# Kernel tuning notes

Measured on AMD Instinct MI355X. Metric: run time of the kernel, lower is better.

Reference implementation:

```python
import jax, jax.numpy as jnp
import numpy as np

H = 16
D_MODEL = 1024
D_K = D_MODEL // H  # 64
NEG = -1e9


def setup_inputs() -> dict:
    key = jax.random.key(0)
    ks = jax.random.split(key, 9)
    nb, nw = 4, 2048
    Q = jax.random.normal(ks[0], (nb, nw, D_MODEL), dtype=jnp.float32)
    K = jax.random.normal(ks[1], (nb, nw, D_MODEL), dtype=jnp.float32)
    V = jax.random.normal(ks[2], (nb, nw, D_MODEL), dtype=jnp.float32)
    mask = jax.random.randint(ks[3], (nb, nw, nw), 0, 2, dtype=jnp.int32)
    s = 1.0 / np.sqrt(D_MODEL)
    Wq = jax.random.normal(ks[4], (D_MODEL, D_MODEL), dtype=jnp.float32) * s
    Wk = jax.random.normal(ks[5], (D_MODEL, D_MODEL), dtype=jnp.float32) * s
    Wv = jax.random.normal(ks[6], (D_MODEL, D_MODEL), dtype=jnp.float32) * s
    Wo = jax.random.normal(ks[7], (D_MODEL, D_MODEL), dtype=jnp.float32) * s
    return {"Q": Q, "K": K, "V": V, "mask": mask,
            "Wq": Wq, "Wk": Wk, "Wv": Wv, "Wo": Wo}


def reference(Q, K, V, mask, Wq, Wk, Wv, Wo):
    nb, nw, _ = Q.shape
    scaling = jnp.asarray(np.sqrt(D_K), dtype=Q.dtype)
    # nn.Linear(bias=False): y = x @ W.T; split heads -> [nb, h, nw, d_k]
    q = (Q @ Wq.T).reshape(nb, nw, H, D_K).transpose(0, 2, 1, 3)
    k = (K @ Wk.T).reshape(nb, nw, H, D_K).transpose(0, 2, 1, 3)
    v = (V @ Wv.T).reshape(nb, nw, H, D_K).transpose(0, 2, 1, 3)
    scores = jnp.einsum('bhqd,bhkd->bhqk', q, k) / scaling
    # mask broadcast over heads (unsqueeze(1) in torch)
    scores = jnp.where(mask[:, None, :, :] == 0, jnp.asarray(NEG, scores.dtype), scores)
    probs = jax.nn.softmax(scores, axis=-1)
    # dropout is identity in eval mode
    attn = jnp.einsum('bhqk,bhkd->bhqd', probs, v)
    x = attn.transpose(0, 2, 1, 3).reshape(nb, nw, D_MODEL)
    return x @ Wo.T
```

## Files before the change

### kernel.cpp

```cpp
#include <hip/hip_runtime.h>
#include <hip/hip_bf16.h>
#include <cstdint>
#include <cmath>

#define NB 4
#define NW 2048
#define DM 1024
#define NH 16
#define DK 64

typedef __attribute__((ext_vector_type(8))) short bf16x8;
typedef __attribute__((ext_vector_type(4))) float f32x4;
union cvt8 { uint4 u; __hip_bfloat16 h[8]; };

__device__ __forceinline__ void async_ld16(const void* g, void* l) {
  __builtin_amdgcn_global_load_lds((__attribute__((address_space(1))) void*)g,
                                   (__attribute__((address_space(3))) void*)l,
                                   16, 0, 0);
}

__device__ __forceinline__ unsigned short bf16bits(float x) {
  __hip_bfloat16 h = __float2bfloat16(x);
  return *(unsigned short*)&h;
}

__global__ void __launch_bounds__(256) cvt_qkv(const float* __restrict__ Q,
                                               const float* __restrict__ K,
                                               const float* __restrict__ V,
                                               __hip_bfloat16* __restrict__ Qb,
                                               __hip_bfloat16* __restrict__ Kb,
                                               __hip_bfloat16* __restrict__ Vb) {
  const float* in = blockIdx.y == 0 ? Q : (blockIdx.y == 1 ? K : V);
  __hip_bfloat16* out = blockIdx.y == 0 ? Qb : (blockIdx.y == 1 ? Kb : Vb);
  size_t i = ((size_t)blockIdx.x * 256 + threadIdx.x) * 8;
  float4 a = *(const float4*)(in + i);
  float4 b = *(const float4*)(in + i + 4);
  cvt8 c;
#pragma unroll
  for (int t = 0; t < 4; ++t) {
    c.h[t]     = __float2bfloat16(((const float*)&a)[t]);
    c.h[4 + t] = __float2bfloat16(((const float*)&b)[t]);
  }
  *(uint4*)(out + i) = c.u;
}

__global__ void __launch_bounds__(256) cvt_w(const float* __restrict__ W0,
                                             const float* __restrict__ W1,
                                             const float* __restrict__ W2,
                                             const float* __restrict__ W3,
                                             __hip_bfloat16* __restrict__ Wb) {
  const float* in = blockIdx.y == 0 ? W0 : (blockIdx.y == 1 ? W1 : (blockIdx.y == 2 ? W2 : W3));
  __hip_bfloat16* out = Wb + (size_t)blockIdx.y * DM * DM;
  size_t i = ((size_t)blockIdx.x * 256 + threadIdx.x) * 8;
  float4 a = *(const float4*)(in + i);
  float4 b = *(const float4*)(in + i + 4);
  cvt8 c;
#pragma unroll
  for (int t = 0; t < 4; ++t) {
    c.h[t]     = __float2bfloat16(((const float*)&a)[t]);
    c.h[4 + t] = __float2bfloat16(((const float*)&b)[t]);
  }
  *(uint4*)(out + i) = c.u;
}

__global__ void __launch_bounds__(256) mask_pack(const int* __restrict__ mask,
                                                 unsigned long long* __restrict__ bits) {
  int lane = threadIdx.x & 63;
  size_t tid = (size_t)blockIdx.x * blockDim.x + threadIdx.x;
  size_t widx = tid >> 6;
  int m = mask[widx * 64 + lane];
  unsigned long long b = __ballot(m != 0);
  if (lane == 0) bits[widx] = b;
}

__global__ void __launch_bounds__(256) gemm_qkv(const __hip_bfloat16* __restrict__ Qb,
                                                const __hip_bfloat16* __restrict__ Kb,
                                                const __hip_bfloat16* __restrict__ Vb,
                                                const __hip_bfloat16* __restrict__ Wb,
                                                __hip_bfloat16* __restrict__ q_ws,
                                                __hip_bfloat16* __restrict__ k_ws,
                                                __hip_bfloat16* __restrict__ vt) {
  __shared__ __align__(16) __hip_bfloat16 sA[128 * 32];
  __shared__ __align__(16) __hip_bfloat16 sB[128 * 32];
  const int z = blockIdx.z;
  const __hip_bfloat16* A = z == 0 ? Qb : (z == 1 ? Kb : Vb);
  const __hip_bfloat16* W = Wb + (size_t)z * DM * DM;
  const int tid = threadIdx.x;
  const int lane = tid & 63;
  const int l15 = lane & 15, quad = lane >> 4;
  const int rowA = blockIdx.y * 128;
  const int colB = blockIdx.x * 128;
  const int wm = ((tid >> 6) >> 1) * 64, wn = ((tid >> 6) & 1) * 64;

  const f32x4 fz = {0.f, 0.f, 0.f, 0.f};
  f32x4 acc[4][4];
#pragma unroll
  for (int i = 0; i < 4; ++i)
#pragma unroll
    for (int j = 0; j < 4; ++j) acc[i][j] = fz;

  for (int k0 = 0; k0 < DM; k0 += 32) {
#pragma unroll
    for (int j = 0; j < 2; ++j) {
      int c = j * 256 + tid;
      int r = c >> 2, col = (c & 3) * 8;
      int ldsOff = (j * 256 + (tid & ~63)) * 16;
      async_ld16(A + (size_t)(rowA + r) * DM + k0 + col, (char*)sA + ldsOff);
      async_ld16(W + (size_t)(colB + r) * DM + k0 + col, (char*)sB + ldsOff);
    }
    __syncthreads();
    bf16x8 af[4], bfr[4];
#pragma unroll
    for (int i = 0; i < 4; ++i) {
      af[i]  = *(const bf16x8*)(sA + (wm + i * 16 + l15) * 32 + quad * 8);
      bfr[i] = *(const bf16x8*)(sB + (wn + i * 16 + l15) * 32 + quad * 8);
    }
#pragma unroll
    for (int i = 0; i < 4; ++i)
#pragma unroll
      for (int j = 0; j < 4; ++j)
        acc[i][j] = __builtin_amdgcn_mfma_f32_16x16x32_bf16(af[i], bfr[j], acc[i][j], 0, 0, 0);
    __syncthreads();
  }

  if (z < 2) {
    __hip_bfloat16* C = z == 0 ? q_ws : k_ws;
    float alpha = z == 0 ? 0.125f : 1.0f;
#pragma unroll
    for (int i = 0; i < 4; ++i) {
      int row = rowA + wm + i * 16 + quad * 4;
#pragma unroll
      for (int j = 0; j < 4; ++j) {
        int col = colB + wn + j * 16 + l15;
#pragma unroll
        for (int r = 0; r < 4; ++r)
          C[(size_t)(row + r) * DM + col] = __float2bfloat16(acc[i][j][r] * alpha);
      }
    }
  } else {
#pragma unroll
    for (int i = 0; i < 4; ++i) {
      int row = rowA + wm + i * 16 + quad * 4;
      int bb = row >> 11, tok = row & 2047;
#pragma unroll
      for (int j = 0; j < 4; ++j) {
        int col = colB + wn + j * 16 + l15;
        uint2 u;
        u.x = (unsigned int)bf16bits(acc[i][j][0]) | ((unsigned int)bf16bits(acc[i][j][1]) << 16);
        u.y = (unsigned int)bf16bits(acc[i][j][2]) | ((unsigned int)bf16bits(acc[i][j][3]) << 16);
        *(uint2*)(vt + ((size_t)bb * 1024 + col) * 2048 + tok) = u;
      }
    }
  }
}

__global__ void __launch_bounds__(256) gemm_out(const __hip_bfloat16* __restrict__ A,
                                                const __hip_bfloat16* __restrict__ W,
                                                float* __restrict__ C) {
  __shared__ __align__(16) __hip_bfloat16 sA[128 * 32];
  __shared__ __align__(16) __hip_bfloat16 sB[128 * 32];
  const int tid = threadIdx.x;
  const int lane = tid & 63;
  const int l15 = lane & 15, quad = lane >> 4;
  const int rowA = blockIdx.y * 128;
  const int colB = blockIdx.x * 128;
  const int wm = ((tid >> 6) >> 1) * 64, wn = ((tid >> 6) & 1) * 64;

  const f32x4 fz = {0.f, 0.f, 0.f, 0.f};
  f32x4 acc[4][4];
#pragma unroll
  for (int i = 0; i < 4; ++i)
#pragma unroll
    for (int j = 0; j < 4; ++j) acc[i][j] = fz;

  for (int k0 = 0; k0 < DM; k0 += 32) {
#pragma unroll
    for (int j = 0; j < 2; ++j) {
      int c = j * 256 + tid;
      int r = c >> 2, col = (c & 3) * 8;
      int ldsOff = (j * 256 + (tid & ~63)) * 16;
      async_ld16(A + (size_t)(rowA + r) * DM + k0 + col, (char*)sA + ldsOff);
      async_ld16(W + (size_t)(colB + r) * DM + k0 + col, (char*)sB + ldsOff);
    }
    __syncthreads();
    bf16x8 af[4], bfr[4];
#pragma unroll
    for (int i = 0; i < 4; ++i) {
      af[i]  = *(const bf16x8*)(sA + (wm + i * 16 + l15) * 32 + quad * 8);
      bfr[i] = *(const bf16x8*)(sB + (wn + i * 16 + l15) * 32 + quad * 8);
    }
#pragma unroll
    for (int i = 0; i < 4; ++i)
#pragma unroll
      for (int j = 0; j < 4; ++j)
        acc[i][j] = __builtin_amdgcn_mfma_f32_16x16x32_bf16(af[i], bfr[j], acc[i][j], 0, 0, 0);
    __syncthreads();
  }
#pragma unroll
  for (int i = 0; i < 4; ++i) {
    int row = rowA + wm + i * 16 + quad * 4;
#pragma unroll
    for (int j = 0; j < 4; ++j) {
      int col = colB + wn + j * 16 + l15;
#pragma unroll
      for (int r = 0; r < 4; ++r)
        C[(size_t)(row + r) * DM + col] = acc[i][j][r];
    }
  }
}

#define LDSK 72

__global__ void __launch_bounds__(256) attn_fused(const __hip_bfloat16* __restrict__ q,
                                                  const __hip_bfloat16* __restrict__ kk,
                                                  const __hip_bfloat16* __restrict__ vt,
                                                  const unsigned long long* __restrict__ mbits,
                                                  __hip_bfloat16* __restrict__ o) {
  __shared__ __align__(16) __hip_bfloat16 sK[64 * LDSK];
  __shared__ __align__(16) __hip_bfloat16 sVT[64 * LDSK];
  __shared__ __align__(16) __hip_bfloat16 sP[4][16 * LDSK];

  const int tid = threadIdx.x;
  const int wave = tid >> 6, lane = tid & 63;
  const int l15 = lane & 15, quad = lane >> 4;
  const int b = blockIdx.z, h = blockIdx.y;
  const int qbase = blockIdx.x * 64 + wave * 16;

  const __hip_bfloat16* qp = q + (size_t)(b * NW + qbase + l15) * DM + h * DK + quad * 8;
  bf16x8 aq0 = *(const bf16x8*)qp;
  bf16x8 aq1 = *(const bf16x8*)(qp + 32);

  const __hip_bfloat16* vbase = vt + ((size_t)b * 1024 + h * DK) * 2048;

  const f32x4 fz = {0.f, 0.f, 0.f, 0.f};
  f32x4 oacc[4];
  float ls[4] = {0.f, 0.f, 0.f, 0.f};
#pragma unroll
  for (int i = 0; i < 4; ++i) oacc[i] = fz;

  for (int kt = 0; kt < NW / 64; ++kt) {
    __syncthreads();
#pragma unroll
    for (int j = 0; j < 2; ++j) {
      int c = j * 256 + tid;
      int r = c >> 3, col = (c & 7) * 8;
      *(uint4*)(sK + r * LDSK + col) =
          *(const uint4*)(kk + (size_t)(b * NW + kt * 64 + r) * DM + h * DK + col);
      *(uint4*)(sVT + r * LDSK + col) =
          *(const uint4*)(vbase + (size_t)r * 2048 + kt * 64 + col);
    }
    unsigned long long mw[4];
#pragma unroll
    for (int r = 0; r < 4; ++r)
      mw[r] = mbits[(size_t)(b * NW + qbase + quad * 4 + r) * (NW / 64) + kt];
    __syncthreads();

    f32x4 S[4];
#pragma unroll
    for (int nc = 0; nc < 4; ++nc) {
      bf16x8 b0 = *(const bf16x8*)(sK + (nc * 16 + l15) * LDSK + quad * 8);
      bf16x8 b1 = *(const bf16x8*)(sK + (nc * 16 + l15) * LDSK + 32 + quad * 8);
      f32x4 t = fz;
      t = __builtin_amdgcn_mfma_f32_16x16x32_bf16(aq0, b0, t, 0, 0, 0);
      t = __builtin_amdgcn_mfma_f32_16x16x32_bf16(aq1, b1, t, 0, 0, 0);
      S[nc] = t;
    }
    unsigned long long sh[4];
#pragma unroll
    for (int r = 0; r < 4; ++r) sh[r] = mw[r] >> l15;
#pragma unroll
    for (int nc = 0; nc < 4; ++nc)
#pragma unroll
      for (int r = 0; r < 4; ++r) {
        float p = __expf(S[nc][r]);
        if (!((sh[r] >> (nc * 16)) & 1ull)) p = 0.f;
        ls[r] += p;
        sP[wave][(quad * 4 + r) * LDSK + nc * 16 + l15] = __float2bfloat16(p);
      }
    __threadfence_block();

    bf16x8 ap0 = *(const bf16x8*)(&sP[wave][l15 * LDSK + quad * 8]);
    bf16x8 ap1 = *(const bf16x8*)(&sP[wave][l15 * LDSK + 32 + quad * 8]);
#pragma unroll
    for (int nc = 0; nc < 4; ++nc) {
      bf16x8 b0 = *(const bf16x8*)(sVT + (nc * 16 + l15) * LDSK + quad * 8);
      bf16x8 b1 = *(const bf16x8*)(sVT + (nc * 16 + l15) * LDSK + 32 + quad * 8);
      oacc[nc] = __builtin_amdgcn_mfma_f32_16x16x32_bf16(ap0, b0, oacc[nc], 0, 0, 0);
      oacc[nc] = __builtin_amdgcn_mfma_f32_16x16x32_bf16(ap1, b1, oacc[nc], 0, 0, 0);
    }
  }

#pragma unroll
  for (int s = 1; s < 16; s <<= 1)
#pragma unroll
    for (int r = 0; r < 4; ++r) ls[r] += __shfl_xor(ls[r], s, 64);

  float inv[4];
#pragma unroll
  for (int r = 0; r < 4; ++r) inv[r] = 1.0f / fmaxf(ls[r], 1e-30f);
#pragma unroll
  for (int nc = 0; nc < 4; ++nc)
#pragma unroll
    for (int r = 0; r < 4; ++r)
      o[(size_t)(b * NW + qbase + quad * 4 + r) * DM + h * DK + nc * 16 + l15] =
          __float2bfloat16(oacc[nc][r] * inv[r]);
}

extern "C" void kernel_launch(void* const* d_in, const int* in_sizes, int n_in,
                              void* d_out, int out_size, void* d_ws, size_t ws_size,
                              hipStream_t stream) {
  const float* Q  = (const float*)d_in[0];
  const float* K  = (const float*)d_in[1];
  const float* V  = (const float*)d_in[2];
  const int*   Mm = (const int*)d_in[3];
  const float* Wq = (const float*)d_in[4];
  const float* Wk = (const float*)d_in[5];
  const float* Wv = (const float*)d_in[6];
  const float* Wo = (const float*)d_in[7];
  float* out = (float*)d_out;

  char* ws = (char*)d_ws;
  const size_t tb = (size_t)NB * NW * DM * sizeof(__hip_bfloat16);
  const size_t wb = (size_t)DM * DM * sizeof(__hip_bfloat16);
  __hip_bfloat16* Qb   = (__hip_bfloat16*)(ws);
  __hip_bfloat16* Kb   = (__hip_bfloat16*)(ws + tb);
  __hip_bfloat16* k_ws = (__hip_bfloat16*)(ws + 2 * tb);
  __hip_bfloat16* vt   = (__hip_bfloat16*)(ws + 3 * tb);
  __hip_bfloat16* Wb   = (__hip_bfloat16*)(ws + 4 * tb);
  unsigned long long* mbits = (unsigned long long*)(ws + 4 * tb + 4 * wb);
  __hip_bfloat16* q_ws = (__hip_bfloat16*)d_out;
  __hip_bfloat16* Vb   = (__hip_bfloat16*)((char*)d_out + tb);
  __hip_bfloat16* a_ws = Qb;

  const int gq = (int)((size_t)NB * NW * DM / 8 / 256);
  const int gw = (int)((size_t)DM * DM / 8 / 256);

  mask_pack<<<(size_t)NB * NW * NW / 256, 256, 0, stream>>>(Mm, mbits);
  cvt_qkv<<<dim3(gq, 3), 256, 0, stream>>>(Q, K, V, Qb, Kb, Vb);
  cvt_w<<<dim3(gw, 4), 256, 0, stream>>>(Wq, Wk, Wv, Wo, Wb);
  gemm_qkv<<<dim3(DM / 128, NB * NW / 128, 3), 256, 0, stream>>>(Qb, Kb, Vb, Wb,
                                                                 q_ws, k_ws, vt);
  attn_fused<<<dim3(NW / 64, NH, NB), 256, 0, stream>>>(q_ws, k_ws, vt, mbits, a_ws);
  gemm_out<<<dim3(DM / 128, NB * NW / 128), 256, 0, stream>>>(a_ws, Wb + 3 * (size_t)DM * DM, out);
}
```

Before: 477.6 us.

## Compute transposed scores and pass P to PV MFMA via permlane swaps instead of LDS

Swaps the MFMA operand order so the S tile comes out transposed, which leaves each lane holding probabilities for one query row. The P fragments for the PV MFMA are then rebuilt in registers with v_permlane32/16_swap, removing the per-wave sP LDS round trip and the fence. The mask bitmap is re-laid out as [b][kt][row] so each lane loads one coalesced word. Exponentials use the native v_exp_f32 with log2(e) folded into the q scaling. The row-sum reduction is restructured to match the new layout, and correctness depends on the permlane lane mapping matching the MFMA A-operand layout.

Measured after the change: 480.2 us. About the same (+0.5%).

```diff
diff --git a/kernel.cpp b/kernel.cpp
--- a/kernel.cpp
+++ b/kernel.cpp
@@ -12,6 +12,7 @@
 typedef __attribute__((ext_vector_type(8))) short bf16x8;
 typedef __attribute__((ext_vector_type(4))) float f32x4;
 union cvt8 { uint4 u; __hip_bfloat16 h[8]; };
+union pk2 { unsigned u; unsigned short s[2]; };
 
 __device__ __forceinline__ void async_ld16(const void* g, void* l) {
   __builtin_amdgcn_global_load_lds((__attribute__((address_space(1))) void*)g,
@@ -22,6 +23,12 @@
 __device__ __forceinline__ unsigned short bf16bits(float x) {
   __hip_bfloat16 h = __float2bfloat16(x);
   return *(unsigned short*)&h;
+}
+
+__device__ __forceinline__ float exp2_fast(float x) {
+  float r;
+  asm("v_exp_f32 %0, %1" : "=v"(r) : "v"(x));
+  return r;
 }
 
 __global__ void __launch_bounds__(256) cvt_qkv(const float* __restrict__ Q,
@@ -69,8 +76,13 @@
   size_t tid = (size_t)blockIdx.x * blockDim.x + threadIdx.x;
   size_t widx = tid >> 6;
   int m = mask[widx * 64 + lane];
-  unsigned long long b = __ballot(m != 0);
-  if (lane == 0) bits[widx] = b;
+  unsigned long long bm = __ballot(m != 0);
+  if (lane == 0) {
+    int kt  = (int)(widx & 31);
+    int row = (int)((widx >> 5) & 2047);
+    int bb  = (int)(widx >> 16);
+    bits[((size_t)bb * 32 + kt) * NW + row] = bm;
+  }
 }
 
 __global__ void __launch_bounds__(256) gemm_qkv(const __hip_bfloat16* __restrict__ Qb,
@@ -125,7 +137,7 @@
 
   if (z < 2) {
     __hip_bfloat16* C = z == 0 ? q_ws : k_ws;
-    float alpha = z == 0 ? 0.125f : 1.0f;
+    float alpha = z == 0 ? 0.18033688011112042f : 1.0f;
 #pragma unroll
     for (int i = 0; i < 4; ++i) {
       int row = rowA + wm + i * 16 + quad * 4;
@@ -214,11 +226,10 @@
 __global__ void __launch_bounds__(256) attn_fused(const __hip_bfloat16* __restrict__ q,
                                                   const __hip_bfloat16* __restrict__ kk,
                                                   const __hip_bfloat16* __restrict__ vt,
-                                                  const unsigned long long* __restrict__ mbits,
+                                                  const unsigned long long* __restrict__ mbt,
                                                   __hip_bfloat16* __restrict__ o) {
   __shared__ __align__(16) __hip_bfloat16 sK[64 * LDSK];
   __shared__ __align__(16) __hip_bfloat16 sVT[64 * LDSK];
-  __shared__ __align__(16) __hip_bfloat16 sP[4][16 * LDSK];
 
   const int tid = threadIdx.x;
   const int wave = tid >> 6, lane = tid & 63;
@@ -231,12 +242,13 @@
   bf16x8 aq1 = *(const bf16x8*)(qp + 32);
 
   const __hip_bfloat16* vbase = vt + ((size_t)b * 1024 + h * DK) * 2048;
+  const unsigned long long* mrow = mbt + (size_t)b * 32 * NW + qbase + l15;
 
   const f32x4 fz = {0.f, 0.f, 0.f, 0.f};
   f32x4 oacc[4];
-  float ls[4] = {0.f, 0.f, 0.f, 0.f};
 #pragma unroll
   for (int i = 0; i < 4; ++i) oacc[i] = fz;
+  float lsr[4] = {0.f, 0.f, 0.f, 0.f};
 
   for (int kt = 0; kt < NW / 64; ++kt) {
     __syncthreads();
@@ -249,55 +261,67 @@
       *(uint4*)(sVT + r * LDSK + col) =
           *(const uint4*)(vbase + (size_t)r * 2048 + kt * 64 + col);
     }
-    unsigned long long mw[4];
-#pragma unroll
-    for (int r = 0; r < 4; ++r)
-      mw[r] = mbits[(size_t)(b * NW + qbase + quad * 4 + r) * (NW / 64) + kt];
-    __syncthreads();
-
-    f32x4 S[4];
+    unsigned long long mw = mrow[(size_t)kt * NW];
+    __syncthreads();
+
+    unsigned long long msh = mw >> (quad * 4);
+    unsigned int u[4][2];
 #pragma unroll
     for (int nc = 0; nc < 4; ++nc) {
-      bf16x8 b0 = *(const bf16x8*)(sK + (nc * 16 + l15) * LDSK + quad * 8);
-      bf16x8 b1 = *(const bf16x8*)(sK + (nc * 16 + l15) * LDSK + 32 + quad * 8);
+      bf16x8 kf0 = *(const bf16x8*)(sK + (nc * 16 + l15) * LDSK + quad * 8);
+      bf16x8 kf1 = *(const bf16x8*)(sK + (nc * 16 + l15) * LDSK + 32 + quad * 8);
       f32x4 t = fz;
-      t = __builtin_amdgcn_mfma_f32_16x16x32_bf16(aq0, b0, t, 0, 0, 0);
-      t = __builtin_amdgcn_mfma_f32_16x16x32_bf16(aq1, b1, t, 0, 0, 0);
-      S[nc] = t;
-    }
-    unsigned long long sh[4];
-#pragma unroll
-    for (int r = 0; r < 4; ++r) sh[r] = mw[r] >> l15;
-#pragma unroll
-    for (int nc = 0; nc < 4; ++nc)
+      t = __builtin_amdgcn_mfma_f32_16x16x32_bf16(kf0, aq0, t, 0, 0, 0);
+      t = __builtin_amdgcn_mfma_f32_16x16x32_bf16(kf1, aq1, t, 0, 0, 0);
+      unsigned nib = (unsigned)(msh >> (nc * 16)) & 0xFu;
+      float p[4];
 #pragma unroll
       for (int r = 0; r < 4; ++r) {
-        float p = __expf(S[nc][r]);
-        if (!((sh[r] >> (nc * 16)) & 1ull)) p = 0.f;
-        ls[r] += p;
-        sP[wave][(quad * 4 + r) * LDSK + nc * 16 + l15] = __float2bfloat16(p);
+        float e = exp2_fast(t[r]);
+        if (!((nib >> r) & 1u)) e = 0.f;
+        lsr[r] += e;
+        p[r] = e;
       }
-    __threadfence_block();
-
-    bf16x8 ap0 = *(const bf16x8*)(&sP[wave][l15 * LDSK + quad * 8]);
-    bf16x8 ap1 = *(const bf16x8*)(&sP[wave][l15 * LDSK + 32 + quad * 8]);
+      pk2 w0; w0.s[0] = bf16bits(p[0]); w0.s[1] = bf16bits(p[1]); u[nc][0] = w0.u;
+      pk2 w1; w1.s[0] = bf16bits(p[2]); w1.s[1] = bf16bits(p[3]); u[nc][1] = w1.u;
+    }
+
+    unsigned a0 = u[0][0], a2 = u[1][0];
+    asm volatile("v_permlane32_swap_b32 %0, %1" : "+v"(a0), "+v"(a2));
+    asm volatile("v_permlane16_swap_b32 %0, %1" : "+v"(a0), "+v"(a2));
+    unsigned a1 = u[0][1], a3 = u[1][1];
+    asm volatile("v_permlane32_swap_b32 %0, %1" : "+v"(a1), "+v"(a3));
+    asm volatile("v_permlane16_swap_b32 %0, %1" : "+v"(a1), "+v"(a3));
+    unsigned c0 = u[2][0], c2 = u[3][0];
+    asm volatile("v_permlane32_swap_b32 %0, %1" : "+v"(c0), "+v"(c2));
+    asm volatile("v_permlane16_swap_b32 %0, %1" : "+v"(c0), "+v"(c2));
+    unsigned c1 = u[2][1], c3 = u[3][1];
+    asm volatile("v_permlane32_swap_b32 %0, %1" : "+v"(c1), "+v"(c3));
+    asm volatile("v_permlane16_swap_b32 %0, %1" : "+v"(c1), "+v"(c3));
+
+    union { unsigned w[4]; bf16x8 v; } AP0, AP1;
+    AP0.w[0] = a0; AP0.w[1] = a1; AP0.w[2] = a2; AP0.w[3] = a3;
+    AP1.w[0] = c0; AP1.w[1] = c1; AP1.w[2] = c2; AP1.w[3] = c3;
+
 #pragma unroll
     for (int nc = 0; nc < 4; ++nc) {
-      bf16x8 b0 = *(const bf16x8*)(sVT + (nc * 16 + l15) * LDSK + quad * 8);
-      bf16x8 b1 = *(const bf16x8*)(sVT + (nc * 16 + l15) * LDSK + 32 + quad * 8);
-      oacc[nc] = __builtin_amdgcn_mfma_f32_16x16x32_bf16(ap0, b0, oacc[nc], 0, 0, 0);
-      oacc[nc] = __builtin_amdgcn_mfma_f32_16x16x32_bf16(ap1, b1, oacc[nc], 0, 0, 0);
-    }
-  }
-
-#pragma unroll
-  for (int s = 1; s < 16; s <<= 1)
-#pragma unroll
-    for (int r = 0; r < 4; ++r) ls[r] += __shfl_xor(ls[r], s, 64);
+      bf16x8 vf0 = *(const bf16x8*)(sVT + (nc * 16 + l15) * LDSK + quad * 8);
+      bf16x8 vf1 = *(const bf16x8*)(sVT + (nc * 16 + l15) * LDSK + 32 + quad * 8);
+      oacc[nc] = __builtin_amdgcn_mfma_f32_16x16x32_bf16(AP0.v, vf0, oacc[nc], 0, 0, 0);
+      oacc[nc] = __builtin_amdgcn_mfma_f32_16x16x32_bf16(AP1.v, vf1, oacc[nc], 0, 0, 0);
+    }
+  }
+
+  float ls = (lsr[0] + lsr[1]) + (lsr[2] + lsr[3]);
+  ls += __shfl_xor(ls, 16, 64);
+  ls += __shfl_xor(ls, 32, 64);
 
   float inv[4];
 #pragma unroll
-  for (int r = 0; r < 4; ++r) inv[r] = 1.0f / fmaxf(ls[r], 1e-30f);
+  for (int r = 0; r < 4; ++r) {
+    float lv = __shfl(ls, quad * 4 + r, 64);
+    inv[r] = 1.0f / fmaxf(lv, 1e-30f);
+  }
 #pragma unroll
   for (int nc = 0; nc < 4; ++nc)
 #pragma unroll
```
